# Kernel tuning notes

Hardware: AMD Instinct MI355X
Metric: run time of the kernel (lower is better)

## Reference

```python
import jax, jax.numpy as jnp
import numpy as np

ROPE_BASE = 10000
B, L, D, NH = 2, 2048, 1024, 16
HD = D // NH


def apply_rope(inputs, positions, base_frequency):
    # inputs: [B, L, N, H], positions: [L]
    head_dim = inputs.shape[-1]
    fraction = 2 * jnp.arange(0, head_dim // 2) / head_dim
    timescale = base_frequency ** fraction  # [H/2]
    sinusoid = positions[..., None] / timescale[None, None, :]  # [1, L, H/2]
    sinusoid = sinusoid[..., None, :]  # [1, L, 1, H/2]
    sin, cos = jnp.sin(sinusoid), jnp.cos(sinusoid)
    first, second = jnp.split(inputs, 2, axis=-1)
    out = jnp.concatenate([first * cos - second * sin,
                           second * cos + first * sin], axis=-1)
    return out.astype(inputs.dtype)


def setup_inputs() -> dict:
    key = jax.random.key(0)
    ks = jax.random.split(key, 5)
    s = 0.02
    return {
        "x": jax.random.normal(ks[0], (B, L, D), jnp.float32),
        "wq_w": jax.random.normal(ks[1], (D, D), jnp.float32) * s,
        "wq_b": jnp.zeros((D,), jnp.float32),
        "wk_w": jax.random.normal(ks[2], (D, D), jnp.float32) * s,
        "wk_b": jnp.zeros((D,), jnp.float32),
        "wv_w": jax.random.normal(ks[3], (D, D), jnp.float32) * s,
        "wv_b": jnp.zeros((D,), jnp.float32),
        "wo_w": jax.random.normal(ks[4], (D, D), jnp.float32) * s,
        "wo_b": jnp.zeros((D,), jnp.float32),
    }


def reference(x, wq_w, wq_b, wk_w, wk_b, wv_w, wv_b, wo_w, wo_b):
    b, l, _ = x.shape
    q = (x @ wq_w + wq_b).reshape(b, l, NH, HD)
    k = (x @ wk_w + wk_b).reshape(b, l, NH, HD)
    v = (x @ wv_w + wv_b).reshape(b, l, NH, HD)
    pos = jnp.arange(l)
    q = apply_rope(q, pos, ROPE_BASE)
    k = apply_rope(k, pos, ROPE_BASE)
    # [B, N, L, H]
    q = q.transpose(0, 2, 1, 3)
    k = k.transpose(0, 2, 1, 3)
    v = v.transpose(0, 2, 1, 3)
    scale = jnp.sqrt(jnp.asarray(HD, q.dtype))
    scores = jnp.einsum('bnqh,bnkh->bnqk', q, k) / scale  # [B, N, L, L]
    causal = jnp.tril(jnp.ones((l, l), bool))
    scores = jnp.where(causal, scores, jnp.finfo(scores.dtype).min)
    attn = jax.nn.softmax(scores, axis=-1)
    ctx = jnp.einsum('bnqk,bnkh->bnqh', attn, v)
    ctx = ctx.transpose(0, 2, 1, 3).reshape(b, l, D)
    return ctx @ wo_w + wo_b
```

## Files before the change

### kernel.cpp

```cpp
#include <hip/hip_runtime.h>
#include <hip/hip_bf16.h>
#include <float.h>
#include <math.h>

#define BB  2
#define LLEN 2048
#define DD  1024
#define NHH 16
#define HDD 64
#define MROWS (BB * LLEN)

typedef __bf16 bf16x8  __attribute__((ext_vector_type(8)));
typedef float  f32x4   __attribute__((ext_vector_type(4)));
typedef float  f32x16  __attribute__((ext_vector_type(16)));
typedef ushort us8     __attribute__((ext_vector_type(8)));

#define EXP2F(x) __builtin_amdgcn_exp2f(x)

static __device__ __forceinline__ ushort f2bf(float f) {
    __hip_bfloat16 h = __float2bfloat16(f);
    return *reinterpret_cast<ushort*>(&h);
}
static __device__ __forceinline__ unsigned pack2(float a, float b) {
    return (unsigned)f2bf(a) | ((unsigned)f2bf(b) << 16);
}

__device__ __forceinline__ void gload16(const void* g, void* l) {
    __builtin_amdgcn_global_load_lds(
        (const __attribute__((address_space(1))) void*)g,
        (__attribute__((address_space(3))) void*)l, 16, 0, 0);
}

__global__ __launch_bounds__(256) void cvt_x_k(const float* __restrict__ in,
                                               ushort* __restrict__ out) {
    int idx = blockIdx.x * 256 + threadIdx.x;
    float4 v = reinterpret_cast<const float4*>(in)[idx];
    ushort4 o;
    o.x = f2bf(v.x); o.y = f2bf(v.y); o.z = f2bf(v.z); o.w = f2bf(v.w);
    reinterpret_cast<ushort4*>(out)[idx] = o;
}

__global__ __launch_bounds__(256) void wt_cvt_all_k(const float* __restrict__ w0,
                                                    const float* __restrict__ w1,
                                                    const float* __restrict__ w2,
                                                    const float* __restrict__ w3,
                                                    ushort* __restrict__ qkv,
                                                    ushort* __restrict__ wo) {
    __shared__ float T[64][65];
    const int z = blockIdx.z;
    const float* in = (z == 0) ? w0 : (z == 1) ? w1 : (z == 2) ? w2 : w3;
    ushort* out = (z < 3) ? (qkv + (size_t)z * 1024 * DD) : wo;

    const int r0 = blockIdx.y * 64, c0 = blockIdx.x * 64;
    const int tid = threadIdx.x;
    for (int i = tid; i < 64 * 16; i += 256) {
        int r = i >> 4, c4 = (i & 15) * 4;
        float4 v = *reinterpret_cast<const float4*>(&in[(size_t)(r0 + r) * DD + c0 + c4]);
        T[r][c4 + 0] = v.x; T[r][c4 + 1] = v.y; T[r][c4 + 2] = v.z; T[r][c4 + 3] = v.w;
    }
    __syncthreads();
    for (int i = tid; i < 64 * 16; i += 256) {
        int rr = i >> 4, cc4 = (i & 15) * 4;
        ushort4 o;
        o.x = f2bf(T[cc4 + 0][rr]);
        o.y = f2bf(T[cc4 + 1][rr]);
        o.z = f2bf(T[cc4 + 2][rr]);
        o.w = f2bf(T[cc4 + 3][rr]);
        *reinterpret_cast<ushort4*>(&out[(size_t)(c0 + rr) * DD + r0 + cc4]) = o;
    }
}

template <int MODE>
__global__ __launch_bounds__(256) void gemm_mfma_k(
    const __bf16* __restrict__ A, const __bf16* __restrict__ Bt,
    const float* __restrict__ bias0, const float* __restrict__ bias1,
    const float* __restrict__ bias2,
    float* __restrict__ out_f32,
    __hip_bfloat16* __restrict__ oq, __hip_bfloat16* __restrict__ ok,
    __hip_bfloat16* __restrict__ ov) {
    constexpr int K = DD;
    __shared__ char smem[32768];
    __bf16* As = (__bf16*)smem;
    __bf16* Bs = As + 128 * 64;

    const int tid  = threadIdx.x;
    const int w    = tid >> 6;
    const int lane = tid & 63;
    const int lr   = lane & 15;
    const int lg   = lane >> 4;
    const int wr   = w >> 1, wc = w & 1;
    const int bm = blockIdx.y * 128, bn = blockIdx.x * 128;

    const int srow = lane >> 3;
    const int scol = ((lane & 7) ^ srow) * 8;
    const __bf16* gA = A  + (size_t)(bm + w * 32 + srow) * K + scol;
    const __bf16* gB = Bt + (size_t)(bn + w * 32 + srow) * K + scol;
    char* ldsA = (char*)As + w * 32 * 128;
    char* ldsB = (char*)Bs + w * 32 * 128;

    f32x4 acc[4][4] = {};

    const int l7 = lr & 7;
    for (int k0 = 0; k0 < K; k0 += 64) {
#pragma unroll
        for (int c = 0; c < 4; ++c) {
            gload16(gA + (size_t)(c * 8) * K + k0, ldsA + c * 1024);
            gload16(gB + (size_t)(c * 8) * K + k0, ldsB + c * 1024);
        }
        __syncthreads();
#pragma unroll
        for (int kk = 0; kk < 2; ++kk) {
            bf16x8 a[4], b[4];
#pragma unroll
            for (int m = 0; m < 4; ++m)
                a[m] = *reinterpret_cast<const bf16x8*>(
                    As + (wr * 64 + m * 16 + lr) * 64 + (((kk * 4 + lg) ^ l7) << 3));
#pragma unroll
            for (int n = 0; n < 4; ++n)
                b[n] = *reinterpret_cast<const bf16x8*>(
                    Bs + (wc * 64 + n * 16 + lr) * 64 + (((kk * 4 + lg) ^ l7) << 3));
#pragma unroll
            for (int m = 0; m < 4; ++m)
#pragma unroll
                for (int n = 0; n < 4; ++n)
                    acc[m][n] = __builtin_amdgcn_mfma_f32_16x16x32_bf16(a[m], b[n], acc[m][n], 0, 0, 0);
        }
        __syncthreads();
    }

    if (MODE == 1) {
        const int seg = bn >> 10;
        const int colbase = (bn & 1023) + wc * 64;
        const int h = colbase >> 6;
        if (seg == 2) {
#pragma unroll
            for (int n = 0; n < 4; ++n) {
                const int hd = n * 16 + lr;
                const float bv = bias2[colbase + hd];
#pragma unroll
                for (int m = 0; m < 4; ++m) {
                    const int rowb = bm + wr * 64 + m * 16 + lg * 4;
                    const int b = rowb >> 11, l0 = rowb & (LLEN - 1);
                    ushort4 st;
                    st.x = f2bf(acc[m][n][0] + bv);
                    st.y = f2bf(acc[m][n][1] + bv);
                    st.z = f2bf(acc[m][n][2] + bv);
                    st.w = f2bf(acc[m][n][3] + bv);
                    const int bh = b * NHH + h;
                    const int t  = l0 >> 5;
                    const int j  = ((hd >> 5) << 1) | ((l0 >> 4) & 1);
                    const int ln = (hd & 31) + ((l0 >> 3) & 1) * 32;
                    const int e0 = l0 & 7;
                    size_t base = ((((size_t)bh * 64 + t) * 4 + j) * 64 + ln) * 8 + e0;
                    *reinterpret_cast<ushort4*>(&ov[base]) = st;
                }
            }
        } else {
            const float* biasp = (seg == 0) ? bias0 : bias1;
            const float osc = (seg == 0) ? 0.18033688011112042f : 1.0f;
            ushort* LP = (ushort*)smem + (size_t)w * 4096;
            __syncthreads();
#pragma unroll
            for (int n2 = 0; n2 < 2; ++n2) {
                const int d = n2 * 16 + lr;
                const float tsd = exp2f((float)d * -0.4152410118609203f);
                const float bv0 = biasp[colbase + d];
                const float bv1 = biasp[colbase + d + 32];
                const int c0  = d >> 4;
                const int hi8 = (d >> 3) & 1;
#pragma unroll
                for (int m = 0; m < 4; ++m) {
#pragma unroll
                    for (int i = 0; i < 4; ++i) {
                        const int lw = m * 16 + lg * 4 + i;
                        const int lglob = (bm & (LLEN - 1)) + wr * 64 + lw;
                        float s, c;
                        __sincosf((float)lglob * tsd, &s, &c);
                        const float x0 = acc[m][n2][i] + bv0;
                        const float x1 = acc[m][n2 + 2][i] + bv1;
                        const int tt = lw >> 5;
                        const int ln = (lw & 31) + 32 * hi8;
                        LP[(((tt << 2) + c0) * 64 + ln) * 8 + (d & 7)] =
                            f2bf((x0 * c - x1 * s) * osc);
                        LP[(((tt << 2) + c0 + 2) * 64 + ln) * 8 + (d & 7)] =
                            f2bf((x1 * c + x0 * s) * osc);
                    }
                }
            }
            __syncthreads();
            ushort* dstp = (ushort*)((seg == 0) ? oq : ok);
            const int bh0 = (bm >> 11) * NHH + h;
            const int tg0 = ((bm & (LLEN - 1)) >> 5) + wr * 2;
#pragma unroll
            for (int tt = 0; tt < 2; ++tt)
#pragma unroll
                for (int c = 0; c < 4; ++c) {
                    us8 v = *reinterpret_cast<const us8*>(
                        &LP[(((tt << 2) + c) * 64 + lane) * 8]);
                    size_t base = ((((size_t)bh0 * 64 + tg0 + tt) * 4 + c) * 64 + lane) * 8;
                    *reinterpret_cast<us8*>(&dstp[base]) = v;
                }
        }
    } else {
        float* FP = (float*)smem + (size_t)w * 2048;
#pragma unroll
        for (int ph = 0; ph < 2; ++ph) {
            __syncthreads();
#pragma unroll
            for (int m2 = 0; m2 < 2; ++m2) {
                const int m = ph * 2 + m2;
#pragma unroll
                for (int n = 0; n < 4; ++n) {
                    const int col = n * 16 + lr;
                    const float bv = bias0[bn + wc * 64 + col];
#pragma unroll
                    for (int i = 0; i < 4; ++i) {
                        const int rw = m2 * 16 + lg * 4 + i;
                        FP[rw * 64 + col] = acc[m][n][i] + bv;
                    }
                }
            }
            __syncthreads();
#pragma unroll
            for (int it = 0; it < 8; ++it) {
                const int idx = it * 64 + lane;
                const int rw = idx >> 4;
                const int cq = idx & 15;
                float4 v = *reinterpret_cast<const float4*>(&FP[rw * 64 + cq * 4]);
                const int row = bm + wr * 64 + ph * 32 + rw;
                *reinterpret_cast<float4*>(
                    &out_f32[(size_t)row * DD + bn + wc * 64 + cq * 4]) = v;
            }
        }
    }
}

#define ATTN_LOAD(KF, VF, T0)                                                   \
    do {                                                                        \
        const __bf16* kp_ = kbase + (size_t)(T0) * 2048;                        \
        KF[0] = *reinterpret_cast<const bf16x8*>(kp_);                          \
        KF[1] = *reinterpret_cast<const bf16x8*>(kp_ + 512);                    \
        KF[2] = *reinterpret_cast<const bf16x8*>(kp_ + 1024);                   \
        KF[3] = *reinterpret_cast<const bf16x8*>(kp_ + 1536);                   \
        const __bf16* vp_ = vbase + (size_t)(T0) * 2048;                        \
        VF[0] = *reinterpret_cast<const bf16x8*>(vp_);                          \
        VF[1] = *reinterpret_cast<const bf16x8*>(vp_ + 512);                    \
        VF[2] = *reinterpret_cast<const bf16x8*>(vp_ + 1024);                   \
        VF[3] = *reinterpret_cast<const bf16x8*>(vp_ + 1536);                   \
    } while (0)

#define ATTN_TILE(KF, VF, T0, MASKIT, QG)                                       \
    do {                                                                        \
        f32x16 s_ = {};                                                         \
        __builtin_amdgcn_s_setprio(1);                                          \
        s_ = __builtin_amdgcn_mfma_f32_32x32x16_bf16(KF[0], qf[0], s_, 0, 0, 0);\
        s_ = __builtin_amdgcn_mfma_f32_32x32x16_bf16(KF[1], qf[1], s_, 0, 0, 0);\
        s_ = __builtin_amdgcn_mfma_f32_32x32x16_bf16(KF[2], qf[2], s_, 0, 0, 0);\
        s_ = __builtin_amdgcn_mfma_f32_32x32x16_bf16(KF[3], qf[3], s_, 0, 0, 0);\
        __builtin_amdgcn_s_setprio(0);                                          \
        float p_[16];                                                           \
        const int k0_ = (T0) * 32;                                              \
        if (MASKIT) {                                                           \
            _Pragma("unroll")                                                   \
            for (int i = 0; i < 16; ++i) {                                      \
                int kkg_ = k0_ + (i & 3) + 8 * (i >> 2) + 4 * hi;               \
                p_[i] = (kkg_ <= (QG)) ? EXP2F(s_[i]) : 0.f;                    \
            }                                                                   \
        } else {                                                                \
            _Pragma("unroll")                                                   \
            for (int i = 0; i < 16; ++i) p_[i] = EXP2F(s_[i]);                  \
        }                                                                       \
        _Pragma("unroll")                                                       \
        for (int i = 0; i < 16; ++i) lsum += p_[i];                             \
        unsigned u_[8], x_[8];                                                  \
        _Pragma("unroll")                                                       \
        for (int j = 0; j < 8; ++j)                                             \
            u_[j] = pack2(p_[2 * j], p_[2 * j + 1]);                            \
        _Pragma("unroll")                                                       \
        for (int j = 0; j < 8; ++j)                                             \
            x_[j] = (unsigned)__shfl_xor((int)u_[j], 32);                       \
        union { unsigned d[4]; bf16x8 v; } B1_, B2_;                            \
        if (hi == 0) {                                                          \
            B1_.d[0] = u_[0]; B1_.d[1] = u_[1]; B1_.d[2] = x_[0]; B1_.d[3] = x_[1]; \
            B2_.d[0] = u_[4]; B2_.d[1] = u_[5]; B2_.d[2] = x_[4]; B2_.d[3] = x_[5]; \
        } else {                                                                \
            B1_.d[0] = x_[2]; B1_.d[1] = x_[3]; B1_.d[2] = u_[2]; B1_.d[3] = u_[3]; \
            B2_.d[0] = x_[6]; B2_.d[1] = x_[7]; B2_.d[2] = u_[6]; B2_.d[3] = u_[7]; \
        }                                                                       \
        __builtin_amdgcn_s_setprio(1);                                          \
        o0 = __builtin_amdgcn_mfma_f32_32x32x16_bf16(VF[0], B1_.v, o0, 0, 0, 0);\
        o0 = __builtin_amdgcn_mfma_f32_32x32x16_bf16(VF[1], B2_.v, o0, 0, 0, 0);\
        o1 = __builtin_amdgcn_mfma_f32_32x32x16_bf16(VF[2], B1_.v, o1, 0, 0, 0);\
        o1 = __builtin_amdgcn_mfma_f32_32x32x16_bf16(VF[3], B2_.v, o1, 0, 0, 0);\
        __builtin_amdgcn_s_setprio(0);                                          \
    } while (0)

#define ATTN_COMPUTE(QT, QG)                                                    \
    do {                                                                        \
        lsum = 0.f;                                                             \
        o0 = (f32x16){}; o1 = (f32x16){};                                       \
        const __bf16* qp_ = qbase + (size_t)(QT) * 2048;                        \
        qf[0] = *reinterpret_cast<const bf16x8*>(qp_);                          \
        qf[1] = *reinterpret_cast<const bf16x8*>(qp_ + 512);                    \
        qf[2] = *reinterpret_cast<const bf16x8*>(qp_ + 1024);                   \
        qf[3] = *reinterpret_cast<const bf16x8*>(qp_ + 1536);                   \
        bf16x8 kf[4], vf[4];                                                    \
        for (int t = w; t <= (QT); t += 4) {                                    \
            ATTN_LOAD(kf, vf, t);                                               \
            ATTN_TILE(kf, vf, t, t == (QT), QG);                                \
        }                                                                       \
    } while (0)

#define ATTN_WRITE_PARTIALS()                                                   \
    do {                                                                        \
        _Pragma("unroll")                                                       \
        for (int r = 0; r < 16; ++r) {                                          \
            oL[w][lane][r]      = o0[r];                                        \
            oL[w][lane][16 + r] = o1[r];                                        \
        }                                                                       \
        lvL[w][lane] = lsum;                                                    \
    } while (0)

#define ATTN_MERGE_WRITE(QG)                                                    \
    do {                                                                        \
        float Lt = 0.f;                                                         \
        _Pragma("unroll")                                                       \
        for (int j = 0; j < 4; ++j)                                             \
            Lt += lvL[j][q32] + lvL[j][q32 + 32];                               \
        const float inv = 1.0f / Lt;                                            \
        __hip_bfloat16* dst = ctx + ((size_t)(b * LLEN + (QG))) * DD + h * HDD; \
        const int T = w >> 1;                                                   \
        const int gb = (w & 1) * 2;                                             \
        _Pragma("unroll")                                                       \
        for (int g2 = 0; g2 < 2; ++g2) {                                        \
            const int g = gb + g2;                                              \
            ushort st4[4];                                                      \
            _Pragma("unroll")                                                   \
            for (int e = 0; e < 4; ++e) {                                       \
                const int r = T * 16 + 4 * g + e;                               \
                float val = oL[0][lane][r] + oL[1][lane][r] +                   \
                            oL[2][lane][r] + oL[3][lane][r];                    \
                st4[e] = f2bf(val * inv);                                       \
            }                                                                   \
            const int d = T * 32 + 8 * g + 4 * hi;                              \
            *reinterpret_cast<ushort4*>(dst + d) =                              \
                *reinterpret_cast<ushort4*>(st4);                               \
        }                                                                       \
    } while (0)

__global__ __launch_bounds__(256) void attn_mfma14_k(const __bf16* __restrict__ Qp,
                                                     const __bf16* __restrict__ Kp,
                                                     const __bf16* __restrict__ Vp,
                                                     __hip_bfloat16* __restrict__ ctx) {
    __shared__ float oL[4][64][33];
    __shared__ float lvL[4][64];

    const int tid  = threadIdx.x;
    const int w    = tid >> 6;
    const int lane = tid & 63;
    const int q32  = lane & 31;
    const int hi   = lane >> 5;

    const int bid = blockIdx.x;
    const int g_  = (bid & 7) * 128 + (bid >> 3);
    const int bh  = g_ >> 5;
    const int ap  = g_ & 31;
    const int qtA = 63 - ap;
    const int qtB = ap;
    const int qgA = qtA * 32 + q32;
    const int qgB = qtB * 32 + q32;

    const __bf16* qbase = Qp + (size_t)bh * (64 * 4 * 512) + lane * 8;
    const __bf16* kbase = Kp + (size_t)bh * (64 * 4 * 512) + lane * 8;
    const __bf16* vbase = Vp + (size_t)bh * (64 * 4 * 512) + lane * 8;

    const int b = bh >> 4, h = bh & 15;

    bf16x8 qf[4];
    f32x16 o0, o1;
    float lsum;

    ATTN_COMPUTE(qtA, qgA);
    ATTN_WRITE_PARTIALS();
    __syncthreads();
    ATTN_MERGE_WRITE(qgA);

    ATTN_COMPUTE(qtB, qgB);
    __syncthreads();
    ATTN_WRITE_PARTIALS();
    __syncthreads();
    ATTN_MERGE_WRITE(qgB);
}

extern "C" void kernel_launch(void* const* d_in, const int* in_sizes, int n_in,
                              void* d_out, int out_size, void* d_ws, size_t ws_size,
                              hipStream_t stream) {
    const float* x    = (const float*)d_in[0];
    const float* wq_w = (const float*)d_in[1];
    const float* wq_b = (const float*)d_in[2];
    const float* wk_w = (const float*)d_in[3];
    const float* wk_b = (const float*)d_in[4];
    const float* wv_w = (const float*)d_in[5];
    const float* wv_b = (const float*)d_in[6];
    const float* wo_w = (const float*)d_in[7];
    const float* wo_b = (const float*)d_in[8];
    float* out = (float*)d_out;

    const size_t MB = 1024 * 1024;
    char* p = (char*)d_ws;
    __bf16* x16   = (__bf16*)p;            p += 8 * MB;
    __bf16* wqkvt = (__bf16*)p;            p += 6 * MB;
    __bf16* wot   = (__bf16*)p;            p += 2 * MB;
    __hip_bfloat16* qp16 = (__hip_bfloat16*)p; p += 8 * MB;
    __hip_bfloat16* kp16 = (__hip_bfloat16*)p; p += 8 * MB;
    __hip_bfloat16* vp16 = (__hip_bfloat16*)p; p += 8 * MB;
    __hip_bfloat16* ctx16 = (__hip_bfloat16*)p;

    hipLaunchKernelGGL(cvt_x_k, dim3(4096), dim3(256), 0, stream, x, (ushort*)x16);
    hipLaunchKernelGGL(wt_cvt_all_k, dim3(16, 16, 4), dim3(256), 0, stream,
                       wq_w, wk_w, wv_w, wo_w, (ushort*)wqkvt, (ushort*)wot);

    hipLaunchKernelGGL((gemm_mfma_k<1>), dim3(24, 32), dim3(256), 0, stream,
                       x16, wqkvt, wq_b, wk_b, wv_b, (float*)nullptr, qp16, kp16, vp16);

    hipLaunchKernelGGL(attn_mfma14_k, dim3(1024), dim3(256), 0, stream,
                       (const __bf16*)qp16, (const __bf16*)kp16, (const __bf16*)vp16, ctx16);

    hipLaunchKernelGGL((gemm_mfma_k<0>), dim3(8, 32), dim3(256), 0, stream,
                       (const __bf16*)ctx16, wot, wo_b, (const float*)nullptr, (const float*)nullptr,
                       out, (__hip_bfloat16*)nullptr, (__hip_bfloat16*)nullptr, (__hip_bfloat16*)nullptr);
}
```

Measured before the change: 109.9 us.

## Double-buffer GEMM LDS tiles with async prefetch of next K-slice

Restructures the projection GEMM main loop to use K-slices of 32 instead of 64, with two LDS buffers. The next slice's global-to-LDS loads are issued before computing on the current one, synchronised through explicit vmcnt waits and raw s_barrier. This is meant to overlap global memory latency with MFMA work, at the cost of twice as many loop iterations and barriers plus a new swizzle pattern that must stay correct.

```diff
diff --git a/kernel.cpp b/kernel.cpp
--- a/kernel.cpp
+++ b/kernel.cpp
@@ -80,8 +80,7 @@
     __hip_bfloat16* __restrict__ ov) {
     constexpr int K = DD;
     __shared__ char smem[32768];
-    __bf16* As = (__bf16*)smem;
-    __bf16* Bs = As + 128 * 64;
+    __bf16* smem_e = (__bf16*)smem;
 
     const int tid  = threadIdx.x;
     const int w    = tid >> 6;
@@ -91,41 +90,58 @@
     const int wr   = w >> 1, wc = w & 1;
     const int bm = blockIdx.y * 128, bn = blockIdx.x * 128;
 
-    const int srow = lane >> 3;
-    const int scol = ((lane & 7) ^ srow) * 8;
-    const __bf16* gA = A  + (size_t)(bm + w * 32 + srow) * K + scol;
-    const __bf16* gB = Bt + (size_t)(bn + w * 32 + srow) * K + scol;
-    char* ldsA = (char*)As + w * 32 * 128;
-    char* ldsB = (char*)Bs + w * 32 * 128;
+    const int srow = lane >> 2;
+    const int schk = (lane & 3) ^ (srow & 3);
+    const __bf16* gA2 = A  + (size_t)(bm + w * 32 + srow) * K + schk * 8;
+    const __bf16* gB2 = Bt + (size_t)(bn + w * 32 + srow) * K + schk * 8;
+    const int ldst = w * 1024 + lane * 8;
 
     f32x4 acc[4][4] = {};
-
-    const int l7 = lr & 7;
-    for (int k0 = 0; k0 < K; k0 += 64) {
-#pragma unroll
-        for (int c = 0; c < 4; ++c) {
-            gload16(gA + (size_t)(c * 8) * K + k0, ldsA + c * 1024);
-            gload16(gB + (size_t)(c * 8) * K + k0, ldsB + c * 1024);
+    const int rchk = (lg ^ (lr & 3)) << 3;
+
+    {
+        __bf16* a_ = smem_e + ldst;
+        gload16(gA2, a_);
+        gload16(gA2 + 16 * (size_t)K, a_ + 512);
+        __bf16* b_ = a_ + 4096;
+        gload16(gB2, b_);
+        gload16(gB2 + 16 * (size_t)K, b_ + 512);
+    }
+
+#pragma unroll 2
+    for (int i = 0; i < 32; ++i) {
+        if (i < 31) {
+            const size_t ko = (size_t)(i + 1) * 32;
+            __bf16* a_ = smem_e + ((i + 1) & 1) * 8192 + ldst;
+            gload16(gA2 + ko, a_);
+            gload16(gA2 + 16 * (size_t)K + ko, a_ + 512);
+            __bf16* b_ = a_ + 4096;
+            gload16(gB2 + ko, b_);
+            gload16(gB2 + 16 * (size_t)K + ko, b_ + 512);
+            asm volatile("s_waitcnt vmcnt(4)" ::: "memory");
+        } else {
+            asm volatile("s_waitcnt vmcnt(0)" ::: "memory");
         }
-        __syncthreads();
-#pragma unroll
-        for (int kk = 0; kk < 2; ++kk) {
-            bf16x8 a[4], b[4];
-#pragma unroll
-            for (int m = 0; m < 4; ++m)
-                a[m] = *reinterpret_cast<const bf16x8*>(
-                    As + (wr * 64 + m * 16 + lr) * 64 + (((kk * 4 + lg) ^ l7) << 3));
+        __builtin_amdgcn_s_barrier();
+        __builtin_amdgcn_sched_barrier(0);
+        const __bf16* As_ = smem_e + (i & 1) * 8192;
+        const __bf16* Bs_ = As_ + 4096;
+        bf16x8 a[4], b[4];
+#pragma unroll
+        for (int m = 0; m < 4; ++m)
+            a[m] = *reinterpret_cast<const bf16x8*>(
+                As_ + (wr * 64 + m * 16 + lr) * 32 + rchk);
+#pragma unroll
+        for (int n = 0; n < 4; ++n)
+            b[n] = *reinterpret_cast<const bf16x8*>(
+                Bs_ + (wc * 64 + n * 16 + lr) * 32 + rchk);
+#pragma unroll
+        for (int m = 0; m < 4; ++m)
 #pragma unroll
             for (int n = 0; n < 4; ++n)
-                b[n] = *reinterpret_cast<const bf16x8*>(
-                    Bs + (wc * 64 + n * 16 + lr) * 64 + (((kk * 4 + lg) ^ l7) << 3));
-#pragma unroll
-            for (int m = 0; m < 4; ++m)
-#pragma unroll
-                for (int n = 0; n < 4; ++n)
-                    acc[m][n] = __builtin_amdgcn_mfma_f32_16x16x32_bf16(a[m], b[n], acc[m][n], 0, 0, 0);
-        }
-        __syncthreads();
+                acc[m][n] = __builtin_amdgcn_mfma_f32_16x16x32_bf16(a[m], b[n], acc[m][n], 0, 0, 0);
+        __builtin_amdgcn_sched_barrier(0);
+        __builtin_amdgcn_s_barrier();
     }
 
     if (MODE == 1) {
```

Result: no change. 110.3 us (+0.4%).

## Give each attention wave its own query tile instead of splitting keys across waves

Applied to the files above, without the earlier changes.

Restructures the attention kernel so each of the four waves in a block owns a distinct 32-row query tile and walks all its key tiles itself, rather than four waves splitting the key range of one tile and merging through shared memory. This removes the LDS partial-output buffers, the block barriers and the cross-wave merge, and halves the grid to 512 blocks with heavy query groups scheduled first. In exchange, waves within a block have unequal work under the causal mask, each wave walks a longer serial key loop, and the paired long/short tile balancing across blocks is gone.

```diff
diff --git a/kernel.cpp b/kernel.cpp
--- a/kernel.cpp
+++ b/kernel.cpp
@@ -295,80 +295,21 @@
         __builtin_amdgcn_s_setprio(0);                                          \
     } while (0)
 
-#define ATTN_COMPUTE(QT, QG)                                                    \
-    do {                                                                        \
-        lsum = 0.f;                                                             \
-        o0 = (f32x16){}; o1 = (f32x16){};                                       \
-        const __bf16* qp_ = qbase + (size_t)(QT) * 2048;                        \
-        qf[0] = *reinterpret_cast<const bf16x8*>(qp_);                          \
-        qf[1] = *reinterpret_cast<const bf16x8*>(qp_ + 512);                    \
-        qf[2] = *reinterpret_cast<const bf16x8*>(qp_ + 1024);                   \
-        qf[3] = *reinterpret_cast<const bf16x8*>(qp_ + 1536);                   \
-        bf16x8 kf[4], vf[4];                                                    \
-        for (int t = w; t <= (QT); t += 4) {                                    \
-            ATTN_LOAD(kf, vf, t);                                               \
-            ATTN_TILE(kf, vf, t, t == (QT), QG);                                \
-        }                                                                       \
-    } while (0)
-
-#define ATTN_WRITE_PARTIALS()                                                   \
-    do {                                                                        \
-        _Pragma("unroll")                                                       \
-        for (int r = 0; r < 16; ++r) {                                          \
-            oL[w][lane][r]      = o0[r];                                        \
-            oL[w][lane][16 + r] = o1[r];                                        \
-        }                                                                       \
-        lvL[w][lane] = lsum;                                                    \
-    } while (0)
-
-#define ATTN_MERGE_WRITE(QG)                                                    \
-    do {                                                                        \
-        float Lt = 0.f;                                                         \
-        _Pragma("unroll")                                                       \
-        for (int j = 0; j < 4; ++j)                                             \
-            Lt += lvL[j][q32] + lvL[j][q32 + 32];                               \
-        const float inv = 1.0f / Lt;                                            \
-        __hip_bfloat16* dst = ctx + ((size_t)(b * LLEN + (QG))) * DD + h * HDD; \
-        const int T = w >> 1;                                                   \
-        const int gb = (w & 1) * 2;                                             \
-        _Pragma("unroll")                                                       \
-        for (int g2 = 0; g2 < 2; ++g2) {                                        \
-            const int g = gb + g2;                                              \
-            ushort st4[4];                                                      \
-            _Pragma("unroll")                                                   \
-            for (int e = 0; e < 4; ++e) {                                       \
-                const int r = T * 16 + 4 * g + e;                               \
-                float val = oL[0][lane][r] + oL[1][lane][r] +                   \
-                            oL[2][lane][r] + oL[3][lane][r];                    \
-                st4[e] = f2bf(val * inv);                                       \
-            }                                                                   \
-            const int d = T * 32 + 8 * g + 4 * hi;                              \
-            *reinterpret_cast<ushort4*>(dst + d) =                              \
-                *reinterpret_cast<ushort4*>(st4);                               \
-        }                                                                       \
-    } while (0)
-
-__global__ __launch_bounds__(256) void attn_mfma14_k(const __bf16* __restrict__ Qp,
+__global__ __launch_bounds__(256) void attn_mfma15_k(const __bf16* __restrict__ Qp,
                                                      const __bf16* __restrict__ Kp,
                                                      const __bf16* __restrict__ Vp,
                                                      __hip_bfloat16* __restrict__ ctx) {
-    __shared__ float oL[4][64][33];
-    __shared__ float lvL[4][64];
-
     const int tid  = threadIdx.x;
     const int w    = tid >> 6;
     const int lane = tid & 63;
     const int q32  = lane & 31;
     const int hi   = lane >> 5;
 
-    const int bid = blockIdx.x;
-    const int g_  = (bid & 7) * 128 + (bid >> 3);
-    const int bh  = g_ >> 5;
-    const int ap  = g_ & 31;
-    const int qtA = 63 - ap;
-    const int qtB = ap;
-    const int qgA = qtA * 32 + q32;
-    const int qgB = qtB * 32 + q32;
+    const int bid  = blockIdx.x;
+    const int bh   = (bid & 7) * 4 + ((bid >> 3) & 3);
+    const int qgrp = 15 - (bid >> 5);
+    const int qt   = qgrp * 4 + w;
+    const int qg   = qt * 32 + q32;
 
     const __bf16* qbase = Qp + (size_t)bh * (64 * 4 * 512) + lane * 8;
     const __bf16* kbase = Kp + (size_t)bh * (64 * 4 * 512) + lane * 8;
@@ -377,19 +318,42 @@
     const int b = bh >> 4, h = bh & 15;
 
     bf16x8 qf[4];
-    f32x16 o0, o1;
-    float lsum;
-
-    ATTN_COMPUTE(qtA, qgA);
-    ATTN_WRITE_PARTIALS();
-    __syncthreads();
-    ATTN_MERGE_WRITE(qgA);
-
-    ATTN_COMPUTE(qtB, qgB);
-    __syncthreads();
-    ATTN_WRITE_PARTIALS();
-    __syncthreads();
-    ATTN_MERGE_WRITE(qgB);
+    const __bf16* qp_ = qbase + (size_t)qt * 2048;
+    qf[0] = *reinterpret_cast<const bf16x8*>(qp_);
+    qf[1] = *reinterpret_cast<const bf16x8*>(qp_ + 512);
+    qf[2] = *reinterpret_cast<const bf16x8*>(qp_ + 1024);
+    qf[3] = *reinterpret_cast<const bf16x8*>(qp_ + 1536);
+
+    f32x16 o0 = {}, o1 = {};
+    float lsum = 0.f;
+
+    bf16x8 kf[4], vf[4];
+    for (int t = 0; t <= qt; ++t) {
+        ATTN_LOAD(kf, vf, t);
+        ATTN_TILE(kf, vf, t, t == qt, qg);
+    }
+
+    float Lt = lsum + __shfl_xor(lsum, 32);
+    const float inv = 1.0f / Lt;
+    __hip_bfloat16* dst = ctx + ((size_t)(b * LLEN + qg)) * DD + h * HDD;
+#pragma unroll
+    for (int g = 0; g < 4; ++g) {
+        ushort4 st;
+        st.x = f2bf(o0[4 * g + 0] * inv);
+        st.y = f2bf(o0[4 * g + 1] * inv);
+        st.z = f2bf(o0[4 * g + 2] * inv);
+        st.w = f2bf(o0[4 * g + 3] * inv);
+        *reinterpret_cast<ushort4*>(dst + 8 * g + 4 * hi) = st;
+    }
+#pragma unroll
+    for (int g = 0; g < 4; ++g) {
+        ushort4 st;
+        st.x = f2bf(o1[4 * g + 0] * inv);
+        st.y = f2bf(o1[4 * g + 1] * inv);
+        st.z = f2bf(o1[4 * g + 2] * inv);
+        st.w = f2bf(o1[4 * g + 3] * inv);
+        *reinterpret_cast<ushort4*>(dst + 32 + 8 * g + 4 * hi) = st;
+    }
 }
 
 extern "C" void kernel_launch(void* const* d_in, const int* in_sizes, int n_in,
@@ -423,7 +387,7 @@
     hipLaunchKernelGGL((gemm_mfma_k<1>), dim3(24, 32), dim3(256), 0, stream,
                        x16, wqkvt, wq_b, wk_b, wv_b, (float*)nullptr, qp16, kp16, vp16);
 
-    hipLaunchKernelGGL(attn_mfma14_k, dim3(1024), dim3(256), 0, stream,
+    hipLaunchKernelGGL(attn_mfma15_k, dim3(512), dim3(256), 0, stream,
                        (const __bf16*)qp16, (const __bf16*)kp16, (const __bf16*)vp16, ctx16);
 
     hipLaunchKernelGGL((gemm_mfma_k<0>), dim3(8, 32), dim3(256), 0, stream,
```

Result: slower. 118.9 us (+8.1%).
